# Optimization experiments

Hardware: AMD Instinct MI355X
Metric: run time of the kernel (lower is better)

Reference implementation:

```python
import jax, jax.numpy as jnp
import numpy as np

B, L, C, K = 32, 512, 256, 3


def conv1d_1ch(sig, w, b):
    # sig: (B, L) single-channel signal; w: (C, 1, K); b: (C,) -> (B, L, C)
    y = jax.lax.conv_general_dilated(
        sig[:, None, :], w, window_strides=(1,), padding=[((K - 1) // 2, (K - 1) // 2)],
        dimension_numbers=('NCH', 'OIH', 'NCH'))  # (B, C, L)
    return y.transpose(0, 2, 1) + b


def setup_inputs() -> dict:
    keys = jax.random.split(jax.random.key(0), 12)
    x = jax.random.normal(keys[0], (B, L, C), dtype=jnp.float32)
    durations_float = jax.random.uniform(keys[1], (B, L), dtype=jnp.float32) * 8.0
    durations_int = jax.random.randint(keys[2], (B, L), 1, 9)
    energies = jax.random.normal(keys[3], (B, L), dtype=jnp.float32)
    pitch = jax.random.normal(keys[4], (B, L), dtype=jnp.float32)
    input_lengths = jax.random.randint(keys[5], (B,), L // 2, L + 1)
    input_lengths = input_lengths.at[0].set(L)  # ensure max_len == L as in torch mask
    Wd = jax.random.normal(keys[6], (C, 1, K), dtype=jnp.float32) * 0.1
    We = jax.random.normal(keys[7], (C, 1, K), dtype=jnp.float32) * 0.1
    Wp = jax.random.normal(keys[8], (C, 1, K), dtype=jnp.float32) * 0.1
    bd = jnp.zeros((C,), jnp.float32)
    be = jnp.zeros((C,), jnp.float32)
    bp = jnp.zeros((C,), jnp.float32)
    Wproj = jax.random.normal(keys[9], (1, C), dtype=jnp.float32) * 0.05
    bproj = jnp.zeros((1,), jnp.float32)
    return dict(x=x, durations_float=durations_float, energies=energies, pitch=pitch,
                Wd=Wd, bd=bd, We=We, be=be, Wp=Wp, bp=bp, Wproj=Wproj, bproj=bproj,
                durations_int=durations_int, input_lengths=input_lengths)


def reference(x, durations_float, energies, pitch, Wd, bd, We, be, Wp, bp, Wproj, bproj,
              durations_int, input_lengths):
    d = conv1d_1ch(durations_float, Wd, bd)   # (B, L, C)
    e = conv1d_1ch(energies, We, be)          # (B, L, C)
    p = conv1d_1ch(pitch, Wp, bp)             # (B, L, C)
    xc = x + e + p                            # x_combined == x_summed (no concatenation)
    range_inputs = xc + d
    ranges = jax.nn.softplus(range_inputs @ Wproj.T + bproj)[..., 0]  # (B, L)

    pad = jnp.arange(L)[None, :] >= input_lengths[:, None]  # True on padding
    ranges = jnp.where(pad, 1.0, ranges)

    cumsum = jnp.cumsum(durations_int, axis=1)
    means = durations_int.astype(jnp.float32) * 0.5
    means = means + jnp.pad(cumsum[:, :-1], ((0, 0), (1, 0))).astype(jnp.float32)  # (B, L)

    T = int(jnp.max(cumsum))
    frames = jnp.arange(T, dtype=jnp.float32) + 0.5  # (T,)

    # Normal(mean, std).log_prob(frames), then exp
    z = (frames[None, None, :] - means[..., None]) / ranges[..., None]  # (B, L, T)
    log_prob = -0.5 * z * z - jnp.log(ranges)[..., None] - 0.5 * jnp.log(2.0 * jnp.pi)
    probs = jnp.exp(log_prob)
    probs = jnp.where(pad[..., None], 0.0, probs)
    weights = probs / (jnp.sum(probs, axis=1, keepdims=True) + 1e-20)  # (B, L, T)

    # sum over L of (B,L,C,T) broadcast-product, done as a batched contraction
    x_upsamp = jnp.einsum('blc,blt->btc', xc, weights)  # (B, T, C)
    return x_upsamp, weights
```

## Files before the change

### kernel.cpp

```cpp
#include <hip/hip_runtime.h>

#define NB 32
#define NL 512
#define NC 256

typedef __attribute__((ext_vector_type(8))) short short8v;
typedef __attribute__((ext_vector_type(4))) float f32x4;

__device__ __forceinline__ unsigned short f2bf(float x) {
    unsigned int u = __float_as_uint(x);
    unsigned int r = (u + 0x7FFFu + ((u >> 16) & 1u)) >> 16;
    return (unsigned short)r;
}

__global__ __launch_bounds__(256) void k_xct(
    const float* __restrict__ x,
    const float* __restrict__ energ, const float* __restrict__ pitch,
    const float* __restrict__ We, const float* __restrict__ be,
    const float* __restrict__ Wp, const float* __restrict__ bp,
    unsigned short* __restrict__ xcT)
{
    __shared__ float se[34], sp[34];
    int lt = blockIdx.x, b = blockIdx.y;
    int c = threadIdx.x;
    int l0 = lt * 32;
    if (c < 34) {
        int gl = l0 - 1 + c;
        bool ok = (gl >= 0) && (gl < NL);
        se[c] = ok ? energ[b*NL + gl] : 0.f;
        sp[c] = ok ? pitch[b*NL + gl] : 0.f;
    }
    __syncthreads();
    float we0 = We[c*3], we1 = We[c*3+1], we2 = We[c*3+2];
    float wp0 = Wp[c*3], wp1 = Wp[c*3+1], wp2 = Wp[c*3+2];
    float bb = be[c] + bp[c];
    const float* xb = x + ((size_t)b*NL + l0)*NC + c;
    unsigned int w32[16];
#pragma unroll
    for (int l = 0; l < 32; ++l) {
        float conv = we0*se[l] + we1*se[l+1] + we2*se[l+2]
                   + wp0*sp[l] + wp1*sp[l+1] + wp2*sp[l+2] + bb;
        float v = xb[(size_t)l*NC] + conv;
        unsigned int bits = f2bf(v);
        if (l & 1) w32[l>>1] |= bits << 16;
        else       w32[l>>1]  = bits;
    }
    uint4* dst = (uint4*)(xcT + ((size_t)(b*16 + lt)*NC + c)*32);
    const uint4* src = (const uint4*)w32;
#pragma unroll
    for (int k = 0; k < 4; ++k) dst[k] = src[k];
}

__global__ __launch_bounds__(256) void k_rdx(
    const float* __restrict__ x, const float* __restrict__ Wproj,
    float* __restrict__ rd)
{
    int blk = blockIdx.x;
    int b = blk >> 7;
    int l = ((blk & 127) << 2) + (threadIdx.x >> 6);
    int lane = threadIdx.x & 63;
    int c0 = lane << 2;
    float4 xv = *(const float4*)(x + ((size_t)(b*NL + l))*NC + c0);
    float4 pw = *(const float4*)(Wproj + c0);
    float dot = xv.x*pw.x + xv.y*pw.y + xv.z*pw.z + xv.w*pw.w;
#pragma unroll
    for (int off = 32; off > 0; off >>= 1) dot += __shfl_down(dot, off, 64);
    if (lane == 0) rd[b*NL + l] = dot;
}

__global__ __launch_bounds__(512) void k_ranges(
    const float* __restrict__ df, const float* __restrict__ energ,
    const float* __restrict__ pitch, const int* __restrict__ di,
    const int* __restrict__ ilen,
    const float* __restrict__ Wd, const float* __restrict__ bd,
    const float* __restrict__ We, const float* __restrict__ be,
    const float* __restrict__ Wp, const float* __restrict__ bp,
    const float* __restrict__ Wproj, const float* __restrict__ bproj,
    const float* __restrict__ rd,
    float* __restrict__ meanO, float* __restrict__ invrO, float* __restrict__ coefO)
{
    __shared__ float red[256];
    __shared__ float pwS[10];
    __shared__ int sbuf[2][NL];
    int b = blockIdx.x;
    int l = threadIdx.x;
    float vals[10];
#pragma unroll
    for (int q = 0; q < 10; ++q) vals[q] = 0.f;
    if (l < 256) {
        float w = Wproj[l];
        vals[0] = Wd[l*3]*w; vals[1] = Wd[l*3+1]*w; vals[2] = Wd[l*3+2]*w;
        vals[3] = We[l*3]*w; vals[4] = We[l*3+1]*w; vals[5] = We[l*3+2]*w;
        vals[6] = Wp[l*3]*w; vals[7] = Wp[l*3+1]*w; vals[8] = Wp[l*3+2]*w;
        vals[9] = (bd[l] + be[l] + bp[l])*w;
    }
#pragma unroll
    for (int q = 0; q < 10; ++q) {
        __syncthreads();
        if (l < 256) red[l] = vals[q];
        __syncthreads();
        for (int off = 128; off > 0; off >>= 1) {
            if (l < off) red[l] += red[l + off];
            __syncthreads();
        }
        if (l == 0) pwS[q] = red[0];
    }

    int d = di[b*NL + l];
    sbuf[0][l] = d;
    __syncthreads();
    int cur = 0;
    for (int off = 1; off < NL; off <<= 1) {
        int v = sbuf[cur][l];
        if (l >= off) v += sbuf[cur][l - off];
        sbuf[cur^1][l] = v;
        __syncthreads();
        cur ^= 1;
    }
    int incl = sbuf[cur][l];
    float mean = (float)incl - 0.5f*(float)d;

    int ro = b*NL + l;
    float fm1 = (l > 0)      ? df[ro-1]    : 0.f;
    float f0  =                df[ro];
    float fp1 = (l < NL-1)   ? df[ro+1]    : 0.f;
    float em1 = (l > 0)      ? energ[ro-1] : 0.f;
    float e0  =                energ[ro];
    float ep1 = (l < NL-1)   ? energ[ro+1] : 0.f;
    float pm1 = (l > 0)      ? pitch[ro-1] : 0.f;
    float p0  =                pitch[ro];
    float pp1 = (l < NL-1)   ? pitch[ro+1] : 0.f;
    float rin = rd[ro]
              + pwS[0]*fm1 + pwS[1]*f0 + pwS[2]*fp1
              + pwS[3]*em1 + pwS[4]*e0 + pwS[5]*ep1
              + pwS[6]*pm1 + pwS[7]*p0 + pwS[8]*pp1
              + pwS[9] + bproj[0];
    float rng = (rin > 20.f) ? rin : log1pf(expf(rin));
    bool pad = (l >= ilen[b]);
    float invr = 1.f / rng;
    meanO[ro] = mean;
    invrO[ro] = pad ? 1.f : invr;
    coefO[ro] = pad ? 0.f : 0.3989422804014327f * invr;
}

__global__ __launch_bounds__(256) void k_denom(
    const float* __restrict__ meanA, const float* __restrict__ invrA,
    const float* __restrict__ coefA, float* __restrict__ dinvA, int T)
{
    __shared__ float red[4][64];
    int b = blockIdx.y;
    int tl = threadIdx.x & 63;
    int part = threadIdx.x >> 6;
    int t = (blockIdx.x << 6) + tl;
    float fr = (float)t + 0.5f;
    const float* mB = meanA + b*NL + part*128;
    const float* iB = invrA + b*NL + part*128;
    const float* cB = coefA + b*NL + part*128;
    float s = 0.f;
#pragma unroll 4
    for (int i = 0; i < 128; ++i) {
        float z = (fr - mB[i]) * iB[i];
        float z2 = z*z;
        s += (z2 < 450.f) ? cB[i]*__expf(-0.5f*z2) : 0.f;
    }
    red[part][tl] = s;
    __syncthreads();
    if (threadIdx.x < 64) {
        float tot = red[0][threadIdx.x] + red[1][threadIdx.x]
                  + red[2][threadIdx.x] + red[3][threadIdx.x];
        int tt = (blockIdx.x << 6) + threadIdx.x;
        if (tt < T) dinvA[(size_t)b*T + tt] = 1.f / (tot + 1e-20f);
    }
}

__global__ __launch_bounds__(256) void k_weights(
    const float* __restrict__ meanA, const float* __restrict__ invrA,
    const float* __restrict__ coefA, const float* __restrict__ dinvA,
    float* __restrict__ outW, int T)
{
    __shared__ float sm[32], si[32], sc[32];
    int lt = blockIdx.x, b = blockIdx.y;
    int l0 = lt*32;
    int tid = threadIdx.x;
    if (tid < 32) {
        sm[tid] = meanA[b*NL + l0 + tid];
        si[tid] = invrA[b*NL + l0 + tid];
        sc[tid] = coefA[b*NL + l0 + tid];
    }
    __syncthreads();
    int nch = (T + 255) >> 8;
    float* ow = outW + (size_t)b*NL*T + (size_t)l0*T;
    for (int ch = 0; ch < nch; ++ch) {
        int t = (ch << 8) + tid;
        bool tok = t < T;
        float dv = tok ? dinvA[(size_t)b*T + t] : 0.f;
        float fr = (float)t + 0.5f;
#pragma unroll
        for (int r = 0; r < 32; ++r) {
            float z = (fr - sm[r]) * si[r];
            float z2 = z*z;
            float p = (z2 < 450.f) ? sc[r]*__expf(-0.5f*z2) : 0.f;
            if (tok) ow[(size_t)r*T + t] = p * dv;
        }
    }
}

__global__ __launch_bounds__(256) void k_gemm(
    const unsigned short* __restrict__ xcT,
    const float* __restrict__ meanA, const float* __restrict__ invrA,
    const float* __restrict__ coefA, const float* __restrict__ dinvA,
    float* __restrict__ outX, int T)
{
    __shared__ __align__(16) unsigned short wT[32 * NL];
    __shared__ unsigned int fl[16];
    int b = blockIdx.y;
    int t0 = blockIdx.x << 5;
    int tid = threadIdx.x;
    int tcol = tid & 31;
    int lbase = tid >> 5;
    if (tid < 16) fl[tid] = 0;
    __syncthreads();

    int t = t0 + tcol;
    float dv = (t < T) ? dinvA[(size_t)b*T + t] : 0.f;
    float fr = (float)t + 0.5f;
    const float* mB = meanA + b*NL;
    const float* iB = invrA + b*NL;
    const float* cB = coefA + b*NL;
    char* wbase = (char*)wT;
    int sw = (tcol & 7) << 4;

#pragma unroll
    for (int i = 0; i < 8; ++i) {
        int ci = lbase + (i << 3);
        int lc = ci << 3;
        const float4 m0  = *(const float4*)(mB + lc);
        const float4 m1  = *(const float4*)(mB + lc + 4);
        const float4 iv0 = *(const float4*)(iB + lc);
        const float4 iv1 = *(const float4*)(iB + lc + 4);
        const float4 cv0 = *(const float4*)(cB + lc);
        const float4 cv1 = *(const float4*)(cB + lc + 4);
        float mm[8] = {m0.x,m0.y,m0.z,m0.w,m1.x,m1.y,m1.z,m1.w};
        float ii[8] = {iv0.x,iv0.y,iv0.z,iv0.w,iv1.x,iv1.y,iv1.z,iv1.w};
        float cc[8] = {cv0.x,cv0.y,cv0.z,cv0.w,cv1.x,cv1.y,cv1.z,cv1.w};
        float w8[8];
        float sum = 0.f;
#pragma unroll
        for (int j = 0; j < 8; ++j) {
            float z = (fr - mm[j]) * ii[j];
            float z2 = z*z;
            float p = (z2 < 450.f) ? cc[j]*__expf(-0.5f*z2) : 0.f;
            float wv2 = p * dv;
            w8[j] = wv2;
            sum += wv2;
        }
        if (sum > 0.f) fl[ci >> 2] = 1u;
        union { unsigned int u[4]; short8v v; } pk;
#pragma unroll
        for (int j = 0; j < 4; ++j)
            pk.u[j] = (unsigned int)f2bf(w8[2*j]) | ((unsigned int)f2bf(w8[2*j+1]) << 16);
        *(short8v*)(wbase + (((tcol << 10) + (ci << 4)) ^ sw)) = pk.v;
    }
    __syncthreads();

    int lane = tid & 63;
    int wvid = tid >> 6;
    int g = lane >> 4;
    int m = lane & 15;
    f32x4 acc[2][4];
#pragma unroll
    for (int mt = 0; mt < 2; ++mt)
#pragma unroll
        for (int nt = 0; nt < 4; ++nt) acc[mt][nt] = (f32x4){0.f,0.f,0.f,0.f};

    const unsigned short* xb = xcT + (size_t)b * 16 * 8192;
    int asw = (m & 7) << 4;

    for (int ks = 0; ks < 16; ++ks) {
        if (fl[ks] == 0u) continue;
        const unsigned short* xk = xb + ks*8192 + g*8;
        short8v a0 = *(const short8v*)(wbase + (((m << 10)      + ks*64 + (g << 4)) ^ asw));
        short8v a1 = *(const short8v*)(wbase + ((((16+m) << 10) + ks*64 + (g << 4)) ^ asw));
#pragma unroll
        for (int nt = 0; nt < 4; ++nt) {
            short8v bf = *(const short8v*)(xk + (size_t)(wvid*64 + nt*16 + m)*32);
            acc[0][nt] = __builtin_amdgcn_mfma_f32_16x16x32_bf16(a0, bf, acc[0][nt], 0, 0, 0);
            acc[1][nt] = __builtin_amdgcn_mfma_f32_16x16x32_bf16(a1, bf, acc[1][nt], 0, 0, 0);
        }
    }

    float* outB = outX + (size_t)b*T*NC + (size_t)(wvid*64 + m);
#pragma unroll
    for (int mt = 0; mt < 2; ++mt) {
#pragma unroll
        for (int r = 0; r < 4; ++r) {
            int tt = t0 + mt*16 + g*4 + r;
            if (tt < T) {
#pragma unroll
                for (int nt = 0; nt < 4; ++nt)
                    outB[(size_t)tt*NC + nt*16] = acc[mt][nt][r];
            }
        }
    }
}

extern "C" void kernel_launch(void* const* d_in, const int* in_sizes, int n_in,
                              void* d_out, int out_size, void* d_ws, size_t ws_size,
                              hipStream_t stream)
{
    const float* x   = (const float*)d_in[0];
    const float* df  = (const float*)d_in[1];
    const float* en  = (const float*)d_in[2];
    const float* pi  = (const float*)d_in[3];
    const float* Wd  = (const float*)d_in[4];
    const float* bd  = (const float*)d_in[5];
    const float* We  = (const float*)d_in[6];
    const float* be  = (const float*)d_in[7];
    const float* Wp  = (const float*)d_in[8];
    const float* bp  = (const float*)d_in[9];
    const float* Wpr = (const float*)d_in[10];
    const float* bpr = (const float*)d_in[11];
    const int*   di  = (const int*)d_in[12];
    const int*   il  = (const int*)d_in[13];

    int T = out_size / (NB * (NC + NL));

    float* outX = (float*)d_out;
    float* outW = outX + (size_t)NB * T * NC;

    float* rdp   = (float*)d_ws;
    float* meanp = rdp   + NB*NL;
    float* invrp = meanp + NB*NL;
    float* coefp = invrp + NB*NL;
    float* dinvp = coefp + NB*NL;
    unsigned short* xcT = (unsigned short*)(dinvp + (size_t)NB*T);

    hipLaunchKernelGGL(k_xct, dim3(16, NB), dim3(256), 0, stream,
                       x, en, pi, We, be, Wp, bp, xcT);
    hipLaunchKernelGGL(k_rdx, dim3(NB*NL/4), dim3(256), 0, stream,
                       x, Wpr, rdp);
    hipLaunchKernelGGL(k_ranges, dim3(NB), dim3(512), 0, stream,
                       df, en, pi, di, il, Wd, bd, We, be, Wp, bp, Wpr, bpr,
                       rdp, meanp, invrp, coefp);
    hipLaunchKernelGGL(k_denom, dim3((T+63)/64, NB), dim3(256), 0, stream,
                       meanp, invrp, coefp, dinvp, T);
    hipLaunchKernelGGL(k_weights, dim3(16, NB), dim3(256), 0, stream,
                       meanp, invrp, coefp, dinvp, outW, T);
    hipLaunchKernelGGL(k_gemm, dim3((T+31)/32, NB), dim3(256), 0, stream,
                       xcT, meanp, invrp, coefp, dinvp, outX, T);
}
```

Before: 332.7 us.

## Fuse denominator, weight output and GEMM into one kernel; fold rd into xct

```diff
diff --git a/kernel.cpp b/kernel.cpp
--- a/kernel.cpp
+++ b/kernel.cpp
@@ -9,8 +9,7 @@
 
 __device__ __forceinline__ unsigned short f2bf(float x) {
     unsigned int u = __float_as_uint(x);
-    unsigned int r = (u + 0x7FFFu + ((u >> 16) & 1u)) >> 16;
-    return (unsigned short)r;
+    return (unsigned short)((u + 0x7FFFu + ((u >> 16) & 1u)) >> 16);
 }
 
 __global__ __launch_bounds__(256) void k_xct(
@@ -18,11 +17,14 @@
     const float* __restrict__ energ, const float* __restrict__ pitch,
     const float* __restrict__ We, const float* __restrict__ be,
     const float* __restrict__ Wp, const float* __restrict__ bp,
-    unsigned short* __restrict__ xcT)
+    const float* __restrict__ Wproj,
+    unsigned short* __restrict__ xcT, float* __restrict__ rd)
 {
     __shared__ float se[34], sp[34];
+    __shared__ float part[4][32];
     int lt = blockIdx.x, b = blockIdx.y;
     int c = threadIdx.x;
+    int lane = c & 63, wv = c >> 6;
     int l0 = lt * 32;
     if (c < 34) {
         int gl = l0 - 1 + c;
@@ -34,6 +36,7 @@
     float we0 = We[c*3], we1 = We[c*3+1], we2 = We[c*3+2];
     float wp0 = Wp[c*3], wp1 = Wp[c*3+1], wp2 = Wp[c*3+2];
     float bb = be[c] + bp[c];
+    float pw = Wproj[c];
     const float* xb = x + ((size_t)b*NL + l0)*NC + c;
     unsigned int w32[16];
 #pragma unroll
@@ -44,71 +47,59 @@
         unsigned int bits = f2bf(v);
         if (l & 1) w32[l>>1] |= bits << 16;
         else       w32[l>>1]  = bits;
+        float contrib = v * pw;
+#pragma unroll
+        for (int off = 32; off > 0; off >>= 1)
+            contrib += __shfl_down(contrib, off, 64);
+        if (lane == 0) part[wv][l] = contrib;
     }
     uint4* dst = (uint4*)(xcT + ((size_t)(b*16 + lt)*NC + c)*32);
     const uint4* src = (const uint4*)w32;
 #pragma unroll
     for (int k = 0; k < 4; ++k) dst[k] = src[k];
-}
-
-__global__ __launch_bounds__(256) void k_rdx(
-    const float* __restrict__ x, const float* __restrict__ Wproj,
-    float* __restrict__ rd)
-{
-    int blk = blockIdx.x;
-    int b = blk >> 7;
-    int l = ((blk & 127) << 2) + (threadIdx.x >> 6);
-    int lane = threadIdx.x & 63;
-    int c0 = lane << 2;
-    float4 xv = *(const float4*)(x + ((size_t)(b*NL + l))*NC + c0);
-    float4 pw = *(const float4*)(Wproj + c0);
-    float dot = xv.x*pw.x + xv.y*pw.y + xv.z*pw.z + xv.w*pw.w;
-#pragma unroll
-    for (int off = 32; off > 0; off >>= 1) dot += __shfl_down(dot, off, 64);
-    if (lane == 0) rd[b*NL + l] = dot;
+    __syncthreads();
+    if (c < 32)
+        rd[b*NL + l0 + c] = part[0][c] + part[1][c] + part[2][c] + part[3][c];
 }
 
 __global__ __launch_bounds__(512) void k_ranges(
-    const float* __restrict__ df, const float* __restrict__ energ,
-    const float* __restrict__ pitch, const int* __restrict__ di,
+    const float* __restrict__ df, const int* __restrict__ di,
     const int* __restrict__ ilen,
     const float* __restrict__ Wd, const float* __restrict__ bd,
-    const float* __restrict__ We, const float* __restrict__ be,
-    const float* __restrict__ Wp, const float* __restrict__ bp,
     const float* __restrict__ Wproj, const float* __restrict__ bproj,
     const float* __restrict__ rd,
     float* __restrict__ meanO, float* __restrict__ invrO, float* __restrict__ coefO)
 {
-    __shared__ float red[256];
-    __shared__ float pwS[10];
+    __shared__ float r2[4][8];
+    __shared__ float pwS[4];
     __shared__ int sbuf[2][NL];
     int b = blockIdx.x;
     int l = threadIdx.x;
-    float vals[10];
-#pragma unroll
-    for (int q = 0; q < 10; ++q) vals[q] = 0.f;
+    int lane = l & 63, wv = l >> 6;
+
+    float vals[4] = {0.f, 0.f, 0.f, 0.f};
     if (l < 256) {
         float w = Wproj[l];
         vals[0] = Wd[l*3]*w; vals[1] = Wd[l*3+1]*w; vals[2] = Wd[l*3+2]*w;
-        vals[3] = We[l*3]*w; vals[4] = We[l*3+1]*w; vals[5] = We[l*3+2]*w;
-        vals[6] = Wp[l*3]*w; vals[7] = Wp[l*3+1]*w; vals[8] = Wp[l*3+2]*w;
-        vals[9] = (bd[l] + be[l] + bp[l])*w;
-    }
-#pragma unroll
-    for (int q = 0; q < 10; ++q) {
-        __syncthreads();
-        if (l < 256) red[l] = vals[q];
-        __syncthreads();
-        for (int off = 128; off > 0; off >>= 1) {
-            if (l < off) red[l] += red[l + off];
-            __syncthreads();
-        }
-        if (l == 0) pwS[q] = red[0];
+        vals[3] = bd[l]*w;
+    }
+#pragma unroll
+    for (int q = 0; q < 4; ++q) {
+        float v = vals[q];
+#pragma unroll
+        for (int off = 32; off > 0; off >>= 1) v += __shfl_down(v, off, 64);
+        if (lane == 0) r2[q][wv] = v;
     }
 
     int d = di[b*NL + l];
     sbuf[0][l] = d;
     __syncthreads();
+    if (l < 4) {
+        float s = 0.f;
+#pragma unroll
+        for (int w8 = 0; w8 < 8; ++w8) s += r2[l][w8];
+        pwS[l] = s;
+    }
     int cur = 0;
     for (int off = 1; off < NL; off <<= 1) {
         int v = sbuf[cur][l];
@@ -121,20 +112,12 @@
     float mean = (float)incl - 0.5f*(float)d;
 
     int ro = b*NL + l;
-    float fm1 = (l > 0)      ? df[ro-1]    : 0.f;
+    float fm1 = (l > 0)      ? df[ro-1] : 0.f;
     float f0  =                df[ro];
-    float fp1 = (l < NL-1)   ? df[ro+1]    : 0.f;
-    float em1 = (l > 0)      ? energ[ro-1] : 0.f;
-    float e0  =                energ[ro];
-    float ep1 = (l < NL-1)   ? energ[ro+1] : 0.f;
-    float pm1 = (l > 0)      ? pitch[ro-1] : 0.f;
-    float p0  =                pitch[ro];
-    float pp1 = (l < NL-1)   ? pitch[ro+1] : 0.f;
+    float fp1 = (l < NL-1)   ? df[ro+1] : 0.f;
     float rin = rd[ro]
               + pwS[0]*fm1 + pwS[1]*f0 + pwS[2]*fp1
-              + pwS[3]*em1 + pwS[4]*e0 + pwS[5]*ep1
-              + pwS[6]*pm1 + pwS[7]*p0 + pwS[8]*pp1
-              + pwS[9] + bproj[0];
+              + pwS[3] + bproj[0];
     float rng = (rin > 20.f) ? rin : log1pf(expf(rin));
     bool pad = (l >= ilen[b]);
     float invr = 1.f / rng;
@@ -143,86 +126,26 @@
     coefO[ro] = pad ? 0.f : 0.3989422804014327f * invr;
 }
 
-__global__ __launch_bounds__(256) void k_denom(
-    const float* __restrict__ meanA, const float* __restrict__ invrA,
-    const float* __restrict__ coefA, float* __restrict__ dinvA, int T)
-{
-    __shared__ float red[4][64];
-    int b = blockIdx.y;
-    int tl = threadIdx.x & 63;
-    int part = threadIdx.x >> 6;
-    int t = (blockIdx.x << 6) + tl;
-    float fr = (float)t + 0.5f;
-    const float* mB = meanA + b*NL + part*128;
-    const float* iB = invrA + b*NL + part*128;
-    const float* cB = coefA + b*NL + part*128;
-    float s = 0.f;
-#pragma unroll 4
-    for (int i = 0; i < 128; ++i) {
-        float z = (fr - mB[i]) * iB[i];
-        float z2 = z*z;
-        s += (z2 < 450.f) ? cB[i]*__expf(-0.5f*z2) : 0.f;
-    }
-    red[part][tl] = s;
-    __syncthreads();
-    if (threadIdx.x < 64) {
-        float tot = red[0][threadIdx.x] + red[1][threadIdx.x]
-                  + red[2][threadIdx.x] + red[3][threadIdx.x];
-        int tt = (blockIdx.x << 6) + threadIdx.x;
-        if (tt < T) dinvA[(size_t)b*T + tt] = 1.f / (tot + 1e-20f);
-    }
-}
-
-__global__ __launch_bounds__(256) void k_weights(
-    const float* __restrict__ meanA, const float* __restrict__ invrA,
-    const float* __restrict__ coefA, const float* __restrict__ dinvA,
-    float* __restrict__ outW, int T)
-{
-    __shared__ float sm[32], si[32], sc[32];
-    int lt = blockIdx.x, b = blockIdx.y;
-    int l0 = lt*32;
-    int tid = threadIdx.x;
-    if (tid < 32) {
-        sm[tid] = meanA[b*NL + l0 + tid];
-        si[tid] = invrA[b*NL + l0 + tid];
-        sc[tid] = coefA[b*NL + l0 + tid];
-    }
-    __syncthreads();
-    int nch = (T + 255) >> 8;
-    float* ow = outW + (size_t)b*NL*T + (size_t)l0*T;
-    for (int ch = 0; ch < nch; ++ch) {
-        int t = (ch << 8) + tid;
-        bool tok = t < T;
-        float dv = tok ? dinvA[(size_t)b*T + t] : 0.f;
-        float fr = (float)t + 0.5f;
-#pragma unroll
-        for (int r = 0; r < 32; ++r) {
-            float z = (fr - sm[r]) * si[r];
-            float z2 = z*z;
-            float p = (z2 < 450.f) ? sc[r]*__expf(-0.5f*z2) : 0.f;
-            if (tok) ow[(size_t)r*T + t] = p * dv;
-        }
-    }
-}
-
-__global__ __launch_bounds__(256) void k_gemm(
+__global__ __launch_bounds__(256) void k_fused(
     const unsigned short* __restrict__ xcT,
     const float* __restrict__ meanA, const float* __restrict__ invrA,
-    const float* __restrict__ coefA, const float* __restrict__ dinvA,
-    float* __restrict__ outX, int T)
+    const float* __restrict__ coefA,
+    float* __restrict__ outX, float* __restrict__ outW, int T)
 {
     __shared__ __align__(16) unsigned short wT[32 * NL];
+    __shared__ float red[8][32];
+    __shared__ float dinvS[32];
     __shared__ unsigned int fl[16];
+
     int b = blockIdx.y;
     int t0 = blockIdx.x << 5;
     int tid = threadIdx.x;
     int tcol = tid & 31;
     int lbase = tid >> 5;
-    if (tid < 16) fl[tid] = 0;
+    if (tid < 16) fl[tid] = 0u;
     __syncthreads();
 
     int t = t0 + tcol;
-    float dv = (t < T) ? dinvA[(size_t)b*T + t] : 0.f;
     float fr = (float)t + 0.5f;
     const float* mB = meanA + b*NL;
     const float* iB = invrA + b*NL;
@@ -230,6 +153,8 @@
     char* wbase = (char*)wT;
     int sw = (tcol & 7) << 4;
 
+    float pv[8][8];
+    float partial = 0.f;
 #pragma unroll
     for (int i = 0; i < 8; ++i) {
         int ci = lbase + (i << 3);
@@ -243,22 +168,46 @@
         float mm[8] = {m0.x,m0.y,m0.z,m0.w,m1.x,m1.y,m1.z,m1.w};
         float ii[8] = {iv0.x,iv0.y,iv0.z,iv0.w,iv1.x,iv1.y,iv1.z,iv1.w};
         float cc[8] = {cv0.x,cv0.y,cv0.z,cv0.w,cv1.x,cv1.y,cv1.z,cv1.w};
-        float w8[8];
         float sum = 0.f;
 #pragma unroll
         for (int j = 0; j < 8; ++j) {
             float z = (fr - mm[j]) * ii[j];
             float z2 = z*z;
             float p = (z2 < 450.f) ? cc[j]*__expf(-0.5f*z2) : 0.f;
-            float wv2 = p * dv;
-            w8[j] = wv2;
-            sum += wv2;
+            pv[i][j] = p;
+            sum += p;
         }
         if (sum > 0.f) fl[ci >> 2] = 1u;
+        partial += sum;
+    }
+    red[lbase][tcol] = partial;
+    __syncthreads();
+    if (tid < 32) {
+        float s = 0.f;
+#pragma unroll
+        for (int g = 0; g < 8; ++g) s += red[g][tid];
+        dinvS[tid] = 1.f / (s + 1e-20f);
+    }
+    __syncthreads();
+    float dv = dinvS[tcol];
+
+    bool tok = t < T;
+    float* ow = outW + (size_t)b*NL*T + t;
+#pragma unroll
+    for (int i = 0; i < 8; ++i) {
+        int ci = lbase + (i << 3);
+        int lc = ci << 3;
         union { unsigned int u[4]; short8v v; } pk;
 #pragma unroll
-        for (int j = 0; j < 4; ++j)
-            pk.u[j] = (unsigned int)f2bf(w8[2*j]) | ((unsigned int)f2bf(w8[2*j+1]) << 16);
+        for (int j = 0; j < 4; ++j) {
+            float w0 = pv[i][2*j]   * dv;
+            float w1 = pv[i][2*j+1] * dv;
+            pk.u[j] = (unsigned int)f2bf(w0) | ((unsigned int)f2bf(w1) << 16);
+            if (tok) {
+                ow[(size_t)(lc + 2*j)   * T] = w0;
+                ow[(size_t)(lc + 2*j+1) * T] = w1;
+            }
+        }
         *(short8v*)(wbase + (((tcol << 10) + (ci << 4)) ^ sw)) = pk.v;
     }
     __syncthreads();
@@ -332,20 +281,12 @@
     float* meanp = rdp   + NB*NL;
     float* invrp = meanp + NB*NL;
     float* coefp = invrp + NB*NL;
-    float* dinvp = coefp + NB*NL;
-    unsigned short* xcT = (unsigned short*)(dinvp + (size_t)NB*T);
+    unsigned short* xcT = (unsigned short*)(coefp + NB*NL);
 
     hipLaunchKernelGGL(k_xct, dim3(16, NB), dim3(256), 0, stream,
-                       x, en, pi, We, be, Wp, bp, xcT);
-    hipLaunchKernelGGL(k_rdx, dim3(NB*NL/4), dim3(256), 0, stream,
-                       x, Wpr, rdp);
+                       x, en, pi, We, be, Wp, bp, Wpr, xcT, rdp);
     hipLaunchKernelGGL(k_ranges, dim3(NB), dim3(512), 0, stream,
-                       df, en, pi, di, il, Wd, bd, We, be, Wp, bp, Wpr, bpr,
-                       rdp, meanp, invrp, coefp);
-    hipLaunchKernelGGL(k_denom, dim3((T+63)/64, NB), dim3(256), 0, stream,
-                       meanp, invrp, coefp, dinvp, T);
-    hipLaunchKernelGGL(k_weights, dim3(16, NB), dim3(256), 0, stream,
-                       meanp, invrp, coefp, dinvp, outW, T);
-    hipLaunchKernelGGL(k_gemm, dim3((T+31)/32, NB), dim3(256), 0, stream,
-                       xcT, meanp, invrp, coefp, dinvp, outX, T);
-}
+                       df, di, il, Wd, bd, Wpr, bpr, rdp, meanp, invrp, coefp);
+    hipLaunchKernelGGL(k_fused, dim3((T+31)/32, NB), dim3(256), 0, stream,
+                       xcT, meanp, invrp, coefp, outX, outW, T);
+}
```

Result: slower. 346.0 us (+4.0%).
